# Kernel optimization log

Hardware: AMD Instinct MI355X
Metric: run time of the kernel (lower is better)

## Reference

```python
import jax, jax.numpy as jnp
import numpy as np

B, S, H = 32, 2048, 1024


def setup_inputs() -> dict:
    key = jax.random.key(0)
    k1, k2, k3, k4, k5, k6 = jax.random.split(key, 6)
    hidden = jax.random.normal(k1, (B, H), dtype=jnp.float32)
    encoder_outputs = jax.random.normal(k2, (B, S, H), dtype=jnp.float32)
    lengths = jax.random.randint(k3, (B,), 1, S + 1, dtype=jnp.int64)
    scale = 1.0 / np.sqrt(H)
    Wq = jax.random.normal(k4, (H, H), dtype=jnp.float32) * scale
    Wk = jax.random.normal(k5, (H, H), dtype=jnp.float32) * scale
    v = jax.random.uniform(k6, (H,), dtype=jnp.float32)  # torch.rand init
    return {"hidden": hidden, "encoder_outputs": encoder_outputs,
            "lengths": lengths, "Wq": Wq, "Wk": Wk, "v": v}


def reference(hidden, encoder_outputs, lengths, Wq, Wk, v):
    # query: (B, 1, H); nn.Linear(bias=False) applies x @ W.T
    query = (hidden @ Wq.T)[:, None, :]
    keys = jnp.einsum('bsh,kh->bsk', encoder_outputs, Wk)  # (B, S, H)
    energy = jnp.tanh(query + keys)                         # (B, S, H)
    attn = jnp.einsum('bsh,h->bs', energy, v)               # (B, S)
    seq = encoder_outputs.shape[1]
    mask = jnp.arange(seq)[None, :] < lengths[:, None]      # (B, S)
    attn = jnp.where(mask, attn, -jnp.inf)
    return jax.nn.softmax(attn, axis=1)
```

## Files before the change

### kernel.cpp

```cpp
#include <hip/hip_runtime.h>
#include <hip/hip_fp16.h>
#include <stdint.h>

#define B_SZ 32
#define S_SZ 2048
#define H_SZ 1024
#define M_SZ (B_SZ * S_SZ)

typedef _Float16 half8 __attribute__((ext_vector_type(8)));
typedef float floatx4 __attribute__((ext_vector_type(4)));

struct h4 { _Float16 x, y, z, w; };

__global__ __launch_bounds__(256) void convert_f32_to_f16(
    const float* __restrict__ in, h4* __restrict__ out, int n4) {
  int i = blockIdx.x * blockDim.x + threadIdx.x;
  int stride = gridDim.x * blockDim.x;
  const float4* in4 = (const float4*)in;
  for (; i < n4; i += stride) {
    float4 f = in4[i];
    h4 o;
    o.x = (_Float16)f.x; o.y = (_Float16)f.y;
    o.z = (_Float16)f.z; o.w = (_Float16)f.w;
    out[i] = o;
  }
}

__global__ __launch_bounds__(256) void query_kernel(
    const float* __restrict__ hidden, const float* __restrict__ Wq,
    float* __restrict__ q) {
  int t = blockIdx.x * blockDim.x + threadIdx.x;
  int b = t & 31;
  int n = t >> 5;
  const float4* h4p = (const float4*)(hidden + (size_t)b * H_SZ);
  const float4* w4p = (const float4*)(Wq + (size_t)n * H_SZ);
  float acc = 0.f;
  #pragma unroll 4
  for (int i = 0; i < H_SZ / 4; ++i) {
    float4 h = h4p[i], w = w4p[i];
    acc = fmaf(h.x, w.x, acc);
    acc = fmaf(h.y, w.y, acc);
    acc = fmaf(h.z, w.z, acc);
    acc = fmaf(h.w, w.w, acc);
  }
  q[(size_t)b * H_SZ + n] = acc;
}

__device__ __forceinline__ void gl_lds16(const void* g, void* l) {
  __builtin_amdgcn_global_load_lds(
      (const __attribute__((address_space(1))) void*)g,
      (__attribute__((address_space(3))) void*)l,
      16, 0, 0);
}

__device__ __forceinline__ float fast_tanh(float x) {
  float ax = fabsf(x);
  float e = __expf(ax * -2.0f);
  float t = (1.0f - e) / (1.0f + e);
  return copysignf(t, x);
}

#define TILE 128
#define BK 32

__global__ __launch_bounds__(256) void fused_keys_kernel(
    const float* __restrict__ A,
    const _Float16* __restrict__ Bt,
    const float* __restrict__ q,
    const float* __restrict__ v,
    float* __restrict__ partial)
{
  __shared__ __align__(16) float    As[2][TILE * BK];
  __shared__ __align__(16) _Float16 Bs[2][TILE * BK];
  __shared__ float q_l[TILE];
  __shared__ float v_l[TILE];

  const int tid  = threadIdx.x;
  const int w    = tid >> 6;
  const int lane = tid & 63;

  const int hw   = blockIdx.x;
  const int xcd  = hw & 7;
  const int slot = hw >> 3;
  const int bn   = slot & 7;
  const int bm   = ((slot >> 3) << 3) | xcd;

  const int R0   = bm * TILE;
  const int C0   = bn * TILE;
  const int bidx = R0 >> 11;

  if (tid < TILE) {
    q_l[tid] = q[(size_t)bidx * H_SZ + C0 + tid];
    v_l[tid] = v[C0 + tid];
  }

  const int cL   = lane & 15, quad = lane >> 4;
  const int sA   = cL >> 1;
  const int sB   = sA & 3;

  floatx4 acc[2][8];
  #pragma unroll
  for (int m = 0; m < 2; ++m)
    #pragma unroll
    for (int n = 0; n < 8; ++n)
      acc[m][n] = (floatx4){0.f, 0.f, 0.f, 0.f};

  const int arow_l = lane >> 3;
  const int ap     = lane & 7;
  const int brow_l = lane >> 2;
  const int bp     = lane & 3;

  const float*    Ablk = A  + (size_t)R0 * H_SZ;
  const _Float16* Bblk = Bt + (size_t)C0 * H_SZ;

  auto stage = [&](int kt2, int b) {
    const int kof = kt2 * BK;
    #pragma unroll
    for (int j = 0; j < 4; ++j) {
      const int row = w * 32 + j * 8 + arow_l;
      const int cg  = ap ^ ((row >> 1) & 7);
      gl_lds16(Ablk + (size_t)row * H_SZ + kof + cg * 4,
               (char*)&As[b][0] + (w * 256 + j * 64) * 16);
    }
    #pragma unroll
    for (int j = 0; j < 2; ++j) {
      const int row = w * 32 + j * 16 + brow_l;
      const int cg  = bp ^ ((row >> 1) & 3);
      gl_lds16(Bblk + (size_t)row * H_SZ + kof + cg * 8,
               (char*)&Bs[b][0] + (w * 128 + j * 64) * 16);
    }
  };

  auto compute = [&](int b) {
    half8 af[2], bf[8];
    #pragma unroll
    for (int m = 0; m < 2; ++m) {
      const int r = w * 32 + m * 16 + cL;
      const float4* Af = (const float4*)&As[b][0] + r * 8;
      float4 f0 = Af[(2 * quad) ^ sA];
      float4 f1 = Af[(2 * quad + 1) ^ sA];
      af[m] = (half8){(_Float16)f0.x, (_Float16)f0.y, (_Float16)f0.z, (_Float16)f0.w,
                      (_Float16)f1.x, (_Float16)f1.y, (_Float16)f1.z, (_Float16)f1.w};
    }
    #pragma unroll
    for (int n = 0; n < 8; ++n) {
      const int r = n * 16 + cL;
      bf[n] = *(const half8*)(&Bs[b][0] + r * 32 + ((quad ^ sB) << 3));
    }
    #pragma unroll
    for (int m = 0; m < 2; ++m)
      #pragma unroll
      for (int n = 0; n < 8; ++n)
        acc[m][n] = __builtin_amdgcn_mfma_f32_16x16x32_f16(af[m], bf[n], acc[m][n], 0, 0, 0);
  };

  stage(0, 0);
  __syncthreads();
  int cur = 0;
  for (int kt = 0; kt < H_SZ / BK - 1; ++kt) {
    stage(kt + 1, cur ^ 1);
    compute(cur);
    __syncthreads();
    cur ^= 1;
  }
  compute(cur);

  float qv[8], vv[8];
  #pragma unroll
  for (int n = 0; n < 8; ++n) {
    const int col = n * 16 + cL;
    qv[n] = q_l[col];
    vv[n] = v_l[col];
  }
  #pragma unroll
  for (int m = 0; m < 2; ++m) {
    #pragma unroll
    for (int r = 0; r < 4; ++r) {
      float s = 0.f;
      #pragma unroll
      for (int n = 0; n < 8; ++n)
        s += vv[n] * fast_tanh(qv[n] + acc[m][n][r]);
      s += __shfl_xor(s, 1);
      s += __shfl_xor(s, 2);
      s += __shfl_xor(s, 4);
      s += __shfl_xor(s, 8);
      if (cL == 0)
        partial[(size_t)bn * M_SZ + R0 + w * 32 + m * 16 + quad * 4 + r] = s;
    }
  }
}

__global__ __launch_bounds__(256) void softmax_kernel(
    const float* __restrict__ partial, const int* __restrict__ lengths,
    float* __restrict__ out) {
  __shared__ float wred[4];
  __shared__ float wsum[4];
  const int b = blockIdx.x;
  const int tid = threadIdx.x;
  const int len = lengths[b];

  float lg[8];
  #pragma unroll
  for (int i = 0; i < 8; ++i) {
    const int s = tid + i * 256;
    const size_t row = (size_t)b * S_SZ + s;
    float l = 0.f;
    #pragma unroll
    for (int nt = 0; nt < 8; ++nt) l += partial[(size_t)nt * M_SZ + row];
    lg[i] = (s < len) ? l : -INFINITY;
  }

  float mx = lg[0];
  #pragma unroll
  for (int i = 1; i < 8; ++i) mx = fmaxf(mx, lg[i]);
  #pragma unroll
  for (int off = 32; off; off >>= 1) mx = fmaxf(mx, __shfl_xor(mx, off));
  if ((tid & 63) == 0) wred[tid >> 6] = mx;
  __syncthreads();
  mx = fmaxf(fmaxf(wred[0], wred[1]), fmaxf(wred[2], wred[3]));

  float pe[8];
  float sum = 0.f;
  #pragma unroll
  for (int i = 0; i < 8; ++i) {
    float e = (lg[i] == -INFINITY) ? 0.f : __expf(lg[i] - mx);
    pe[i] = e;
    sum += e;
  }
  #pragma unroll
  for (int off = 32; off; off >>= 1) sum += __shfl_xor(sum, off);
  if ((tid & 63) == 0) wsum[tid >> 6] = sum;
  __syncthreads();
  sum = wsum[0] + wsum[1] + wsum[2] + wsum[3];
  const float inv = 1.0f / sum;

  #pragma unroll
  for (int i = 0; i < 8; ++i) {
    const int s = tid + i * 256;
    out[(size_t)b * S_SZ + s] = pe[i] * inv;
  }
}

extern "C" void kernel_launch(void* const* d_in, const int* in_sizes, int n_in,
                              void* d_out, int out_size, void* d_ws, size_t ws_size,
                              hipStream_t stream) {
  const float* hidden  = (const float*)d_in[0];
  const float* enc     = (const float*)d_in[1];
  const int*   lengths = (const int*)d_in[2];
  const float* Wq      = (const float*)d_in[3];
  const float* Wk      = (const float*)d_in[4];
  const float* v       = (const float*)d_in[5];
  float* out = (float*)d_out;

  char* ws = (char*)d_ws;
  _Float16* B16     = (_Float16*)ws;
  float*    q       = (float*)(ws + 2097152);
  float*    partial = (float*)(ws + 2097152 + 131072);

  convert_f32_to_f16<<<1024, 256, 0, stream>>>(Wk, (h4*)B16, (H_SZ * H_SZ) / 4);
  query_kernel<<<128, 256, 0, stream>>>(hidden, Wq, q);
  fused_keys_kernel<<<(M_SZ / TILE) * (H_SZ / TILE), 256, 0, stream>>>(enc, B16, q, v, partial);
  softmax_kernel<<<B_SZ, 256, 0, stream>>>(partial, lengths, out);
}
```

Before: 620.6 us.

## Stage fp32 A tile through registers and store it to LDS as fp16

The encoder-output tile no longer goes from global memory straight into LDS as fp32. It is loaded into registers, converted to fp16, and written to a swizzled fp16 LDS buffer after the MFMA compute of the current stage. This halves the LDS footprint and read traffic for A and removes the per-iteration conversion inside compute. It also adds a launch-bounds occupancy hint of 4 blocks per CU. The cost is extra registers to hold the prefetched A data, which could cause spills under the tighter register budget.

```diff
diff --git a/kernel.cpp b/kernel.cpp
--- a/kernel.cpp
+++ b/kernel.cpp
@@ -63,14 +63,14 @@
 #define TILE 128
 #define BK 32
 
-__global__ __launch_bounds__(256) void fused_keys_kernel(
+__global__ __launch_bounds__(256, 4) void fused_keys_kernel(
     const float* __restrict__ A,
     const _Float16* __restrict__ Bt,
     const float* __restrict__ q,
     const float* __restrict__ v,
     float* __restrict__ partial)
 {
-  __shared__ __align__(16) float    As[2][TILE * BK];
+  __shared__ __align__(16) _Float16 As[2][TILE * BK];
   __shared__ __align__(16) _Float16 Bs[2][TILE * BK];
   __shared__ float q_l[TILE];
   __shared__ float v_l[TILE];
@@ -95,8 +95,7 @@
   }
 
   const int cL   = lane & 15, quad = lane >> 4;
-  const int sA   = cL >> 1;
-  const int sB   = sA & 3;
+  const int sB   = (cL >> 1) & 3;
 
   floatx4 acc[2][8];
   #pragma unroll
@@ -105,23 +104,19 @@
     for (int n = 0; n < 8; ++n)
       acc[m][n] = (floatx4){0.f, 0.f, 0.f, 0.f};
 
-  const int arow_l = lane >> 3;
-  const int ap     = lane & 7;
+  const int arow = w * 32 + (lane >> 1);
+  const int ah   = lane & 1;
+  const int akey = (lane >> 2) & 3;
+  const int ap0  = (2 * ah)     ^ akey;
+  const int ap1  = (2 * ah + 1) ^ akey;
+  const float* Asrc = A + (size_t)(R0 + arow) * H_SZ + ah * 16;
+
   const int brow_l = lane >> 2;
   const int bp     = lane & 3;
-
-  const float*    Ablk = A  + (size_t)R0 * H_SZ;
   const _Float16* Bblk = Bt + (size_t)C0 * H_SZ;
 
-  auto stage = [&](int kt2, int b) {
+  auto stageB = [&](int kt2, int b) {
     const int kof = kt2 * BK;
-    #pragma unroll
-    for (int j = 0; j < 4; ++j) {
-      const int row = w * 32 + j * 8 + arow_l;
-      const int cg  = ap ^ ((row >> 1) & 7);
-      gl_lds16(Ablk + (size_t)row * H_SZ + kof + cg * 4,
-               (char*)&As[b][0] + (w * 256 + j * 64) * 16);
-    }
     #pragma unroll
     for (int j = 0; j < 2; ++j) {
       const int row = w * 32 + j * 16 + brow_l;
@@ -131,21 +126,33 @@
     }
   };
 
+  float4 ar[4];
+  auto loadA = [&](int kt2) {
+    const float4* p = (const float4*)(Asrc + kt2 * BK);
+    ar[0] = p[0]; ar[1] = p[1]; ar[2] = p[2]; ar[3] = p[3];
+  };
+
+  auto writeA = [&](int b) {
+    half8 h0 = (half8){(_Float16)ar[0].x, (_Float16)ar[0].y, (_Float16)ar[0].z, (_Float16)ar[0].w,
+                       (_Float16)ar[1].x, (_Float16)ar[1].y, (_Float16)ar[1].z, (_Float16)ar[1].w};
+    half8 h1 = (half8){(_Float16)ar[2].x, (_Float16)ar[2].y, (_Float16)ar[2].z, (_Float16)ar[2].w,
+                       (_Float16)ar[3].x, (_Float16)ar[3].y, (_Float16)ar[3].z, (_Float16)ar[3].w};
+    _Float16* dst = &As[b][arow * BK];
+    *(half8*)(dst + ap0 * 8) = h0;
+    *(half8*)(dst + ap1 * 8) = h1;
+  };
+
   auto compute = [&](int b) {
     half8 af[2], bf[8];
     #pragma unroll
     for (int m = 0; m < 2; ++m) {
       const int r = w * 32 + m * 16 + cL;
-      const float4* Af = (const float4*)&As[b][0] + r * 8;
-      float4 f0 = Af[(2 * quad) ^ sA];
-      float4 f1 = Af[(2 * quad + 1) ^ sA];
-      af[m] = (half8){(_Float16)f0.x, (_Float16)f0.y, (_Float16)f0.z, (_Float16)f0.w,
-                      (_Float16)f1.x, (_Float16)f1.y, (_Float16)f1.z, (_Float16)f1.w};
+      af[m] = *(const half8*)(&As[b][r * BK] + ((quad ^ sB) << 3));
     }
     #pragma unroll
     for (int n = 0; n < 8; ++n) {
       const int r = n * 16 + cL;
-      bf[n] = *(const half8*)(&Bs[b][0] + r * 32 + ((quad ^ sB) << 3));
+      bf[n] = *(const half8*)(&Bs[b][r * BK] + ((quad ^ sB) << 3));
     }
     #pragma unroll
     for (int m = 0; m < 2; ++m)
@@ -154,12 +161,17 @@
         acc[m][n] = __builtin_amdgcn_mfma_f32_16x16x32_f16(af[m], bf[n], acc[m][n], 0, 0, 0);
   };
 
-  stage(0, 0);
+  loadA(0);
+  stageB(0, 0);
+  writeA(0);
   __syncthreads();
+
   int cur = 0;
   for (int kt = 0; kt < H_SZ / BK - 1; ++kt) {
-    stage(kt + 1, cur ^ 1);
+    loadA(kt + 1);
+    stageB(kt + 1, cur ^ 1);
     compute(cur);
+    writeA(cur ^ 1);
     __syncthreads();
     cur ^= 1;
   }
```

Result: no change. 610.0 us (-1.7%).
